# Kernel tuning notes

Hardware: AMD Instinct MI355X
Metric: run time of the kernel (lower is better)

## Reference

```python
import jax, jax.numpy as jnp
import numpy as np

B, S, E, H = 8, 2048, 384, 6
D = E // H  # head dim = 64


def setup_inputs() -> dict:
    key = jax.random.key(0)
    ks = jax.random.split(key, 5)
    s = 1.0 / np.sqrt(E)
    return {
        "x": jax.random.normal(ks[0], (B, S, E), dtype=jnp.float32),
        "Wq": jax.random.normal(ks[1], (E, E), dtype=jnp.float32) * s,
        "Wk": jax.random.normal(ks[2], (E, E), dtype=jnp.float32) * s,
        "Wv": jax.random.normal(ks[3], (E, E), dtype=jnp.float32) * s,
        "Wo": jax.random.normal(ks[4], (E, E), dtype=jnp.float32) * s,
        "bo": jnp.zeros((E,), dtype=jnp.float32),
    }


def reference(x, Wq, Wk, Wv, Wo, bo):
    b, s, e = x.shape
    # QKV projections (torch Linear with bias=False: x @ W.T; here W stored as [in,out])
    q = (x @ Wq).reshape(b, s, H, D).transpose(0, 2, 1, 3)  # [b,h,s,d]
    k = (x @ Wk).reshape(b, s, H, D).transpose(0, 2, 1, 3)
    v = (x @ Wv).reshape(b, s, H, D).transpose(0, 2, 1, 3)
    scores = jnp.einsum("bhqd,bhkd->bhqk", q, k) / jnp.sqrt(jnp.asarray(D, x.dtype))
    causal = jnp.tril(jnp.ones((s, s), dtype=bool))
    scores = jnp.where(causal, scores, -jnp.inf)
    attn = jax.nn.softmax(scores, axis=-1)
    # NOTE: original applies dropout but then uses the PRE-dropout softmax for @V,
    # so dropout is a no-op; we faithfully omit it.
    out = jnp.einsum("bhqk,bhkd->bhqd", attn, v)  # [b,h,s,d]
    out = out.transpose(0, 2, 1, 3).reshape(b, s, e)
    return out @ Wo + bo
```

## Files before the change

kernel.cpp:

```cpp
#include <hip/hip_runtime.h>
#include <hip/hip_bf16.h>
#include <cstdint>
#include <cstddef>

typedef __attribute__((ext_vector_type(8))) short short8;
typedef __attribute__((ext_vector_type(4))) float f32x4;

#define S_LEN 2048
#define EMB 384
#define NH 6
#define HD 64
#define NB 8
#define QSCALE 0.180336880f

__device__ __forceinline__ unsigned short f2bf(float f) {
  return __builtin_bit_cast(unsigned short, __float2bfloat16(f));
}

__global__ __launch_bounds__(256) void k_prep(
    const float* __restrict__ x, unsigned short* __restrict__ xb,
    const float* __restrict__ Wq, const float* __restrict__ Wk,
    const float* __restrict__ Wv, const float* __restrict__ Wo,
    unsigned short* __restrict__ Wqt, unsigned short* __restrict__ Wkt,
    unsigned short* __restrict__ Wvt, unsigned short* __restrict__ Wot) {
  const int tid = threadIdx.x;
  if (blockIdx.x < 1536) {
    int i = blockIdx.x * 256 + tid;
    const int n4 = (NB * S_LEN * EMB) / 4;
    for (; i < n4; i += 1536 * 256) {
      const float4 v = reinterpret_cast<const float4*>(x)[i];
      ushort4 o;
      o.x = f2bf(v.x); o.y = f2bf(v.y); o.z = f2bf(v.z); o.w = f2bf(v.w);
      reinterpret_cast<ushort4*>(xb)[i] = o;
    }
  } else {
    __shared__ unsigned short Lw[64 * 66];
    const int bx2 = blockIdx.x - 1536;
    const int mat = bx2 / 36;
    const int tile = bx2 - mat * 36;
    const int k0 = (tile / 6) * 64;
    const int n0 = (tile % 6) * 64;
    const float* W = (mat == 0) ? Wq : (mat == 1) ? Wk : (mat == 2) ? Wv : Wo;
    unsigned short* Wt = (mat == 0) ? Wqt : (mat == 1) ? Wkt : (mat == 2) ? Wvt : Wot;
    const int f4 = tid & 15;
#pragma unroll
    for (int it = 0; it < 4; ++it) {
      const int kl = it * 16 + (tid >> 4);
      const float4 v = reinterpret_cast<const float4*>(W + (size_t)(k0 + kl) * EMB + n0)[f4];
      Lw[kl * 66 + f4 * 4 + 0] = f2bf(v.x);
      Lw[kl * 66 + f4 * 4 + 1] = f2bf(v.y);
      Lw[kl * 66 + f4 * 4 + 2] = f2bf(v.z);
      Lw[kl * 66 + f4 * 4 + 3] = f2bf(v.w);
    }
    __syncthreads();
    const int g = tid & 7;
#pragma unroll
    for (int it = 0; it < 2; ++it) {
      const int nl = it * 32 + (tid >> 3);
      short8 o;
#pragma unroll
      for (int j = 0; j < 8; ++j) o[j] = (short)Lw[(g * 8 + j) * 66 + nl];
      *reinterpret_cast<short8*>(Wt + (size_t)(n0 + nl) * EMB + k0 + g * 8) = o;
    }
  }
}

__global__ __launch_bounds__(256) void k_qkv(
    const unsigned short* __restrict__ xb,
    const unsigned short* __restrict__ Wqt,
    const unsigned short* __restrict__ Wkt,
    const unsigned short* __restrict__ Wvt,
    unsigned short* __restrict__ Qb,
    unsigned short* __restrict__ Kb,
    unsigned short* __restrict__ Vtb) {
  __shared__ __attribute__((aligned(16))) unsigned short La[128 * 72];
  __shared__ __attribute__((aligned(16))) unsigned short Lt[64 * 136];

  const int tid = threadIdx.x;
  const int lane = tid & 63;
  const int w = tid >> 6;
  const int wr = w >> 1, wc = w & 1;
  const int lr = lane & 15, lg = lane >> 4;

  const int bid = blockIdx.y * 128 + blockIdx.x;
  const int xcd = bid & 7;
  const int pos = bid >> 3;
  const int bx = xcd * 16 + (pos & 15);
  const int by = pos >> 4;
  const int m0 = bx * 128;
  const int wsel = by / 3;
  const int n0 = (by % 3) * 128;
  const unsigned short* Wt = (wsel == 0) ? Wqt : (wsel == 1) ? Wkt : Wvt;

  const int srow = tid >> 3;
  const int sg = tid & 7;

  f32x4 acc[4][4] = {};
  short8 st[4];
  short8 breg[2][2][4];

#pragma unroll
  for (int i = 0; i < 4; ++i)
    st[i] = *reinterpret_cast<const short8*>(
        xb + (size_t)(m0 + i * 32 + srow) * EMB + sg * 8);
#pragma unroll
  for (int kk = 0; kk < 2; ++kk)
#pragma unroll
    for (int ns = 0; ns < 4; ++ns)
      breg[0][kk][ns] = *reinterpret_cast<const short8*>(
          Wt + (size_t)(n0 + wc * 64 + ns * 16 + lr) * EMB + kk * 32 + lg * 8);

#pragma unroll
  for (int kt = 0; kt < 6; ++kt) {
    const int cur = kt & 1, nxt = cur ^ 1;
    __syncthreads();
#pragma unroll
    for (int i = 0; i < 4; ++i)
      *reinterpret_cast<short8*>(&La[(i * 32 + srow) * 72 + sg * 8]) = st[i];
    __syncthreads();
    if (kt < 5) {
      const int kn = (kt + 1) * 64;
#pragma unroll
      for (int i = 0; i < 4; ++i)
        st[i] = *reinterpret_cast<const short8*>(
            xb + (size_t)(m0 + i * 32 + srow) * EMB + kn + sg * 8);
#pragma unroll
      for (int kk = 0; kk < 2; ++kk)
#pragma unroll
        for (int ns = 0; ns < 4; ++ns)
          breg[nxt][kk][ns] = *reinterpret_cast<const short8*>(
              Wt + (size_t)(n0 + wc * 64 + ns * 16 + lr) * EMB + kn + kk * 32 + lg * 8);
    }
#pragma unroll
    for (int kk = 0; kk < 2; ++kk) {
      short8 a[4];
#pragma unroll
      for (int ms = 0; ms < 4; ++ms)
        a[ms] = *reinterpret_cast<const short8*>(
            &La[(wr * 64 + ms * 16 + lr) * 72 + kk * 32 + lg * 8]);
#pragma unroll
      for (int ms = 0; ms < 4; ++ms)
#pragma unroll
        for (int ns = 0; ns < 4; ++ns)
          acc[ms][ns] = __builtin_amdgcn_mfma_f32_16x16x32_bf16(
              a[ms], breg[cur][kk][ns], acc[ms][ns], 0, 0, 0);
    }
  }

  if (wsel != 2) {
    unsigned short* Out = (wsel == 0) ? Qb : Kb;
    const float sc = (wsel == 0) ? QSCALE : 1.0f;
#pragma unroll
    for (int ms = 0; ms < 4; ++ms)
#pragma unroll
      for (int ns = 0; ns < 4; ++ns)
#pragma unroll
        for (int r = 0; r < 4; ++r) {
          const int m = m0 + wr * 64 + ms * 16 + lg * 4 + r;
          const int n = n0 + wc * 64 + ns * 16 + lr;
          const int bb = m >> 11;
          const int s = m & 2047;
          const int h = n >> 6;
          const int d = n & 63;
          Out[(((size_t)bb * NH + h) * S_LEN + s) * HD + d] = f2bf(acc[ms][ns][r] * sc);
        }
  } else {
    const int bb = m0 >> 11;
    const int s0 = m0 & 2047;
#pragma unroll
    for (int p = 0; p < 2; ++p) {
      __syncthreads();
      if (wc == p) {
#pragma unroll
        for (int ms = 0; ms < 4; ++ms)
#pragma unroll
          for (int ns = 0; ns < 4; ++ns)
#pragma unroll
            for (int r = 0; r < 4; ++r) {
              const int dl = ns * 16 + lr;
              const int ml = wr * 64 + ms * 16 + lg * 4 + r;
              Lt[dl * 136 + (((ml >> 3) ^ (dl & 7)) << 3) + (ml & 7)] = f2bf(acc[ms][ns][r]);
            }
      }
      __syncthreads();
      const int hg = 2 * (n0 >> 7) + p;
      const int c = tid & 15;
#pragma unroll
      for (int it = 0; it < 4; ++it) {
        const int d = it * 16 + (tid >> 4);
        const short8 v = *reinterpret_cast<const short8*>(
            &Lt[d * 136 + ((c ^ (d & 7)) << 3)]);
        *reinterpret_cast<short8*>(
            Vtb + (((size_t)bb * NH + hg) * HD + d) * S_LEN + s0 + c * 8) = v;
      }
    }
  }
}

__global__ __launch_bounds__(256) void k_attn(
    const unsigned short* __restrict__ Qb,
    const unsigned short* __restrict__ Kb,
    const unsigned short* __restrict__ Vtg,
    unsigned short* __restrict__ Ob) {
  __shared__ __attribute__((aligned(16))) unsigned short Ks[64 * 64];
  __shared__ __attribute__((aligned(16))) unsigned short Vt[64 * 64];
  __shared__ __attribute__((aligned(16))) unsigned short Ps[64 * 64];

  const int tid = threadIdx.x;
  const int lane = tid & 63;
  const int w = tid >> 6;
  const int lr = lane & 15, lg = lane >> 4;

  const int lin = blockIdx.y * 16 + blockIdx.x;
  const int swz = (lin & 7) * 96 + (lin >> 3);
  const int pair = swz & 15;
  const int bh = swz >> 4;

  const unsigned short* Qp = Qb + (size_t)bh * S_LEN * HD;
  const unsigned short* Kp = Kb + (size_t)bh * S_LEN * HD;
  const unsigned short* Vp = Vtg + (size_t)bh * S_LEN * HD;
  const int b = bh / NH, hh = bh - b * NH;

  const int srow = tid >> 3;
  const int sslot = tid & 7;
  const int wsl0 = (sslot ^ (srow & 7)) << 3;

  for (int phase = 0; phase < 2; ++phase) {
    const int qt = phase ? (31 - pair) : pair;
    const int qbase = qt * 64 + w * 16;

    const short8 aq0 = *reinterpret_cast<const short8*>(Qp + (size_t)(qbase + lr) * HD + lg * 8);
    const short8 aq1 = *reinterpret_cast<const short8*>(Qp + (size_t)(qbase + lr) * HD + 32 + lg * 8);

    f32x4 o[4] = {};
    float l_i[4] = {0.f, 0.f, 0.f, 0.f};

    short8 pk0 = *reinterpret_cast<const short8*>(Kp + (size_t)srow * HD + sslot * 8);
    short8 pk1 = *reinterpret_cast<const short8*>(Kp + (size_t)(srow + 32) * HD + sslot * 8);
    short8 pv0 = *reinterpret_cast<const short8*>(Vp + (size_t)srow * S_LEN + sslot * 8);
    short8 pv1 = *reinterpret_cast<const short8*>(Vp + (size_t)(srow + 32) * S_LEN + sslot * 8);

    for (int t = 0; t <= qt; ++t) {
      __syncthreads();
      *reinterpret_cast<short8*>(&Ks[srow * 64 + wsl0]) = pk0;
      *reinterpret_cast<short8*>(&Ks[(srow + 32) * 64 + wsl0]) = pk1;
      *reinterpret_cast<short8*>(&Vt[srow * 64 + wsl0]) = pv0;
      *reinterpret_cast<short8*>(&Vt[(srow + 32) * 64 + wsl0]) = pv1;
      __syncthreads();

      if (t < qt) {
        const int tn = (t + 1) * 64;
        pk0 = *reinterpret_cast<const short8*>(Kp + (size_t)(tn + srow) * HD + sslot * 8);
        pk1 = *reinterpret_cast<const short8*>(Kp + (size_t)(tn + srow + 32) * HD + sslot * 8);
        pv0 = *reinterpret_cast<const short8*>(Vp + (size_t)srow * S_LEN + tn + sslot * 8);
        pv1 = *reinterpret_cast<const short8*>(Vp + (size_t)(srow + 32) * S_LEN + tn + sslot * 8);
      }

      float sv[4][4];
#pragma unroll
      for (int ks = 0; ks < 4; ++ks) {
        const int kstart = t * 64 + ks * 16;
        if (kstart > qbase + 15) {
#pragma unroll
          for (int r = 0; r < 4; ++r) sv[ks][r] = -1e30f;
        } else {
          const int krow = ks * 16 + lr;
          const int kx = krow & 7;
          const short8 bk0 = *reinterpret_cast<const short8*>(&Ks[krow * 64 + ((lg ^ kx) << 3)]);
          const short8 bk1 = *reinterpret_cast<const short8*>(&Ks[krow * 64 + (((4 + lg) ^ kx) << 3)]);
          f32x4 s = {};
          s = __builtin_amdgcn_mfma_f32_16x16x32_bf16(aq0, bk0, s, 0, 0, 0);
          s = __builtin_amdgcn_mfma_f32_16x16x32_bf16(aq1, bk1, s, 0, 0, 0);
          if (kstart + 15 <= qbase) {
#pragma unroll
            for (int r = 0; r < 4; ++r) sv[ks][r] = s[r];
          } else {
            const int kg = kstart + lr;
#pragma unroll
            for (int r = 0; r < 4; ++r)
              sv[ks][r] = (kg <= qbase + lg * 4 + r) ? s[r] : -1e30f;
          }
        }
      }

#pragma unroll
      for (int r = 0; r < 4; ++r) {
        const int q = w * 16 + lg * 4 + r;
        const int qx = q & 7;
        const int abase = q * 64 + (lr & 7);
        const int sp = lr >> 3;
        float p[4];
#pragma unroll
        for (int ks = 0; ks < 4; ++ks) p[ks] = __builtin_amdgcn_exp2f(sv[ks][r]);
        l_i[r] += (p[0] + p[1]) + (p[2] + p[3]);
#pragma unroll
        for (int ks = 0; ks < 4; ++ks)
          Ps[abase + ((((ks << 1) | sp) ^ qx) << 3)] = f2bf(p[ks]);
      }

      const int qrow = w * 16 + lr;
      const int qx2 = qrow & 7;
#pragma unroll
      for (int kk = 0; kk < 2; ++kk) {
        const short8 ap = *reinterpret_cast<const short8*>(
            &Ps[qrow * 64 + (((kk * 4 + lg) ^ qx2) << 3)]);
#pragma unroll
        for (int ns = 0; ns < 4; ++ns) {
          const int vrow = ns * 16 + lr;
          const short8 bv = *reinterpret_cast<const short8*>(
              &Vt[vrow * 64 + (((kk * 4 + lg) ^ (vrow & 7)) << 3)]);
          o[ns] = __builtin_amdgcn_mfma_f32_16x16x32_bf16(ap, bv, o[ns], 0, 0, 0);
        }
      }
    }

#pragma unroll
    for (int r = 0; r < 4; ++r) {
      float l = l_i[r];
      l += __shfl_xor(l, 1);
      l += __shfl_xor(l, 2);
      l += __shfl_xor(l, 4);
      l += __shfl_xor(l, 8);
      l_i[r] = 1.0f / l;
    }
#pragma unroll
    for (int ns = 0; ns < 4; ++ns)
#pragma unroll
      for (int r = 0; r < 4; ++r) {
        const int qg = qbase + lg * 4 + r;
        const float val = o[ns][r] * l_i[r];
        Ob[((size_t)(b * S_LEN + qg)) * EMB + hh * HD + ns * 16 + lr] = f2bf(val);
      }
  }
}

__global__ __launch_bounds__(256) void k_oproj(
    const unsigned short* __restrict__ Ob,
    const unsigned short* __restrict__ Wot,
    const float* __restrict__ bo,
    float* __restrict__ out) {
  __shared__ __attribute__((aligned(16))) unsigned short La[64 * 72];

  const int tid = threadIdx.x;
  const int lane = tid & 63;
  const int w = tid >> 6;
  const int lr = lane & 15, lg = lane >> 4;

  const int bid = blockIdx.y * 256 + blockIdx.x;
  const int xcd = bid & 7;
  const int pos = bid >> 3;
  const int m0 = (xcd * 32 + (pos & 31)) * 64;
  const int n0 = (pos >> 5) * 128;

  const int srow = tid >> 3;
  const int sg = tid & 7;

  f32x4 acc[4][2] = {};
  short8 st[2];
  short8 breg[2][2][2];

#pragma unroll
  for (int i = 0; i < 2; ++i)
    st[i] = *reinterpret_cast<const short8*>(
        Ob + (size_t)(m0 + i * 32 + srow) * EMB + sg * 8);
#pragma unroll
  for (int kk = 0; kk < 2; ++kk)
#pragma unroll
    for (int ns = 0; ns < 2; ++ns)
      breg[0][kk][ns] = *reinterpret_cast<const short8*>(
          Wot + (size_t)(n0 + w * 32 + ns * 16 + lr) * EMB + kk * 32 + lg * 8);

#pragma unroll
  for (int kt = 0; kt < 6; ++kt) {
    const int cur = kt & 1, nxt = cur ^ 1;
    __syncthreads();
#pragma unroll
    for (int i = 0; i < 2; ++i)
      *reinterpret_cast<short8*>(&La[(i * 32 + srow) * 72 + sg * 8]) = st[i];
    __syncthreads();
    if (kt < 5) {
      const int kn = (kt + 1) * 64;
#pragma unroll
      for (int i = 0; i < 2; ++i)
        st[i] = *reinterpret_cast<const short8*>(
            Ob + (size_t)(m0 + i * 32 + srow) * EMB + kn + sg * 8);
#pragma unroll
      for (int kk = 0; kk < 2; ++kk)
#pragma unroll
        for (int ns = 0; ns < 2; ++ns)
          breg[nxt][kk][ns] = *reinterpret_cast<const short8*>(
              Wot + (size_t)(n0 + w * 32 + ns * 16 + lr) * EMB + kn + kk * 32 + lg * 8);
    }
#pragma unroll
    for (int kk = 0; kk < 2; ++kk) {
      short8 a[4];
#pragma unroll
      for (int ms = 0; ms < 4; ++ms)
        a[ms] = *reinterpret_cast<const short8*>(
            &La[(ms * 16 + lr) * 72 + kk * 32 + lg * 8]);
#pragma unroll
      for (int ms = 0; ms < 4; ++ms)
#pragma unroll
        for (int ns = 0; ns < 2; ++ns)
          acc[ms][ns] = __builtin_amdgcn_mfma_f32_16x16x32_bf16(
              a[ms], breg[cur][kk][ns], acc[ms][ns], 0, 0, 0);
    }
  }

#pragma unroll
  for (int ms = 0; ms < 4; ++ms)
#pragma unroll
    for (int ns = 0; ns < 2; ++ns)
#pragma unroll
      for (int r = 0; r < 4; ++r) {
        const int m = m0 + ms * 16 + lg * 4 + r;
        const int n = n0 + w * 32 + ns * 16 + lr;
        out[(size_t)m * EMB + n] = acc[ms][ns][r] + bo[n];
      }
}

extern "C" void kernel_launch(void* const* d_in, const int* in_sizes, int n_in,
                              void* d_out, int out_size, void* d_ws, size_t ws_size,
                              hipStream_t stream) {
  const float* x  = (const float*)d_in[0];
  const float* Wq = (const float*)d_in[1];
  const float* Wk = (const float*)d_in[2];
  const float* Wv = (const float*)d_in[3];
  const float* Wo = (const float*)d_in[4];
  const float* bo = (const float*)d_in[5];
  float* out = (float*)d_out;

  uint8_t* ws = (uint8_t*)d_ws;
  unsigned short* xb  = (unsigned short*)(ws);
  unsigned short* Wqt = (unsigned short*)(ws + 12582912);
  unsigned short* Wkt = (unsigned short*)(ws + 12877824);
  unsigned short* Wvt = (unsigned short*)(ws + 13172736);
  unsigned short* Wot = (unsigned short*)(ws + 13467648);
  unsigned short* Qb  = (unsigned short*)(ws + 13762560);
  unsigned short* Kb  = (unsigned short*)(ws + 26345472);
  unsigned short* VT  = (unsigned short*)(ws + 38928384);
  unsigned short* Ob  = (unsigned short*)(ws + 51511296);

  hipLaunchKernelGGL(k_prep, dim3(1680), dim3(256), 0, stream,
                     x, xb, Wq, Wk, Wv, Wo, Wqt, Wkt, Wvt, Wot);
  hipLaunchKernelGGL(k_qkv, dim3(128, 9), dim3(256), 0, stream,
                     xb, Wqt, Wkt, Wvt, Qb, Kb, VT);
  hipLaunchKernelGGL(k_attn, dim3(16, 48), dim3(256), 0, stream, Qb, Kb, VT, Ob);
  hipLaunchKernelGGL(k_oproj, dim3(256, 3), dim3(256), 0, stream, Ob, Wot, bo, out);
}
```

Measured before the change: 197.8 us.

## Fuse x bf16 conversion into QKV GEMM and stage epilogue stores through LDS

Removes the separate pass that converted x to bf16 into a workspace buffer. The QKV GEMM now loads fp32 x directly and converts it while staging into LDS, and the prep kernel only transposes the weights. The Q/K epilogue and the output projection epilogue now write through shared memory so each thread issues wide, coalesced vector stores instead of scattered scalar ones. In exchange, fp32 x is re-read by each of the 9 column blocks, which doubles the bytes per load, and the extra LDS buffer in k_oproj may lower occupancy.

```diff
diff --git a/kernel.cpp b/kernel.cpp
--- a/kernel.cpp
+++ b/kernel.cpp
@@ -17,56 +17,44 @@
   return __builtin_bit_cast(unsigned short, __float2bfloat16(f));
 }
 
-__global__ __launch_bounds__(256) void k_prep(
-    const float* __restrict__ x, unsigned short* __restrict__ xb,
+__global__ __launch_bounds__(256) void k_prepw(
     const float* __restrict__ Wq, const float* __restrict__ Wk,
     const float* __restrict__ Wv, const float* __restrict__ Wo,
     unsigned short* __restrict__ Wqt, unsigned short* __restrict__ Wkt,
     unsigned short* __restrict__ Wvt, unsigned short* __restrict__ Wot) {
+  __shared__ unsigned short Lw[64 * 66];
   const int tid = threadIdx.x;
-  if (blockIdx.x < 1536) {
-    int i = blockIdx.x * 256 + tid;
-    const int n4 = (NB * S_LEN * EMB) / 4;
-    for (; i < n4; i += 1536 * 256) {
-      const float4 v = reinterpret_cast<const float4*>(x)[i];
-      ushort4 o;
-      o.x = f2bf(v.x); o.y = f2bf(v.y); o.z = f2bf(v.z); o.w = f2bf(v.w);
-      reinterpret_cast<ushort4*>(xb)[i] = o;
-    }
-  } else {
-    __shared__ unsigned short Lw[64 * 66];
-    const int bx2 = blockIdx.x - 1536;
-    const int mat = bx2 / 36;
-    const int tile = bx2 - mat * 36;
-    const int k0 = (tile / 6) * 64;
-    const int n0 = (tile % 6) * 64;
-    const float* W = (mat == 0) ? Wq : (mat == 1) ? Wk : (mat == 2) ? Wv : Wo;
-    unsigned short* Wt = (mat == 0) ? Wqt : (mat == 1) ? Wkt : (mat == 2) ? Wvt : Wot;
-    const int f4 = tid & 15;
-#pragma unroll
-    for (int it = 0; it < 4; ++it) {
-      const int kl = it * 16 + (tid >> 4);
-      const float4 v = reinterpret_cast<const float4*>(W + (size_t)(k0 + kl) * EMB + n0)[f4];
-      Lw[kl * 66 + f4 * 4 + 0] = f2bf(v.x);
-      Lw[kl * 66 + f4 * 4 + 1] = f2bf(v.y);
-      Lw[kl * 66 + f4 * 4 + 2] = f2bf(v.z);
-      Lw[kl * 66 + f4 * 4 + 3] = f2bf(v.w);
-    }
-    __syncthreads();
-    const int g = tid & 7;
-#pragma unroll
-    for (int it = 0; it < 2; ++it) {
-      const int nl = it * 32 + (tid >> 3);
-      short8 o;
-#pragma unroll
-      for (int j = 0; j < 8; ++j) o[j] = (short)Lw[(g * 8 + j) * 66 + nl];
-      *reinterpret_cast<short8*>(Wt + (size_t)(n0 + nl) * EMB + k0 + g * 8) = o;
-    }
+  const int bx2 = blockIdx.x;
+  const int mat = bx2 / 36;
+  const int tile = bx2 - mat * 36;
+  const int k0 = (tile / 6) * 64;
+  const int n0 = (tile % 6) * 64;
+  const float* W = (mat == 0) ? Wq : (mat == 1) ? Wk : (mat == 2) ? Wv : Wo;
+  unsigned short* Wt = (mat == 0) ? Wqt : (mat == 1) ? Wkt : (mat == 2) ? Wvt : Wot;
+  const int f4 = tid & 15;
+#pragma unroll
+  for (int it = 0; it < 4; ++it) {
+    const int kl = it * 16 + (tid >> 4);
+    const float4 v = reinterpret_cast<const float4*>(W + (size_t)(k0 + kl) * EMB + n0)[f4];
+    Lw[kl * 66 + f4 * 4 + 0] = f2bf(v.x);
+    Lw[kl * 66 + f4 * 4 + 1] = f2bf(v.y);
+    Lw[kl * 66 + f4 * 4 + 2] = f2bf(v.z);
+    Lw[kl * 66 + f4 * 4 + 3] = f2bf(v.w);
+  }
+  __syncthreads();
+  const int g = tid & 7;
+#pragma unroll
+  for (int it = 0; it < 2; ++it) {
+    const int nl = it * 32 + (tid >> 3);
+    short8 o;
+#pragma unroll
+    for (int j = 0; j < 8; ++j) o[j] = (short)Lw[(g * 8 + j) * 66 + nl];
+    *reinterpret_cast<short8*>(Wt + (size_t)(n0 + nl) * EMB + k0 + g * 8) = o;
   }
 }
 
 __global__ __launch_bounds__(256) void k_qkv(
-    const unsigned short* __restrict__ xb,
+    const float* __restrict__ x,
     const unsigned short* __restrict__ Wqt,
     const unsigned short* __restrict__ Wkt,
     const unsigned short* __restrict__ Wvt,
@@ -96,13 +84,15 @@
   const int sg = tid & 7;
 
   f32x4 acc[4][4] = {};
-  short8 st[4];
+  float4 xf[4][2];
   short8 breg[2][2][4];
 
 #pragma unroll
-  for (int i = 0; i < 4; ++i)
-    st[i] = *reinterpret_cast<const short8*>(
-        xb + (size_t)(m0 + i * 32 + srow) * EMB + sg * 8);
+  for (int i = 0; i < 4; ++i) {
+    const float* src = x + (size_t)(m0 + i * 32 + srow) * EMB + sg * 8;
+    xf[i][0] = *reinterpret_cast<const float4*>(src);
+    xf[i][1] = *reinterpret_cast<const float4*>(src + 4);
+  }
 #pragma unroll
   for (int kk = 0; kk < 2; ++kk)
 #pragma unroll
@@ -115,15 +105,23 @@
     const int cur = kt & 1, nxt = cur ^ 1;
     __syncthreads();
 #pragma unroll
-    for (int i = 0; i < 4; ++i)
-      *reinterpret_cast<short8*>(&La[(i * 32 + srow) * 72 + sg * 8]) = st[i];
+    for (int i = 0; i < 4; ++i) {
+      short8 v;
+      v[0] = (short)f2bf(xf[i][0].x); v[1] = (short)f2bf(xf[i][0].y);
+      v[2] = (short)f2bf(xf[i][0].z); v[3] = (short)f2bf(xf[i][0].w);
+      v[4] = (short)f2bf(xf[i][1].x); v[5] = (short)f2bf(xf[i][1].y);
+      v[6] = (short)f2bf(xf[i][1].z); v[7] = (short)f2bf(xf[i][1].w);
+      *reinterpret_cast<short8*>(&La[(i * 32 + srow) * 72 + sg * 8]) = v;
+    }
     __syncthreads();
     if (kt < 5) {
       const int kn = (kt + 1) * 64;
 #pragma unroll
-      for (int i = 0; i < 4; ++i)
-        st[i] = *reinterpret_cast<const short8*>(
-            xb + (size_t)(m0 + i * 32 + srow) * EMB + kn + sg * 8);
+      for (int i = 0; i < 4; ++i) {
+        const float* src = x + (size_t)(m0 + i * 32 + srow) * EMB + kn + sg * 8;
+        xf[i][0] = *reinterpret_cast<const float4*>(src);
+        xf[i][1] = *reinterpret_cast<const float4*>(src + 4);
+      }
 #pragma unroll
       for (int kk = 0; kk < 2; ++kk)
 #pragma unroll
@@ -147,26 +145,37 @@
     }
   }
 
+  const int bb = m0 >> 11;
+  const int s0 = m0 & 2047;
   if (wsel != 2) {
     unsigned short* Out = (wsel == 0) ? Qb : Kb;
     const float sc = (wsel == 0) ? QSCALE : 1.0f;
 #pragma unroll
-    for (int ms = 0; ms < 4; ++ms)
-#pragma unroll
-      for (int ns = 0; ns < 4; ++ns)
-#pragma unroll
-        for (int r = 0; r < 4; ++r) {
-          const int m = m0 + wr * 64 + ms * 16 + lg * 4 + r;
-          const int n = n0 + wc * 64 + ns * 16 + lr;
-          const int bb = m >> 11;
-          const int s = m & 2047;
-          const int h = n >> 6;
-          const int d = n & 63;
-          Out[(((size_t)bb * NH + h) * S_LEN + s) * HD + d] = f2bf(acc[ms][ns][r] * sc);
-        }
+    for (int p = 0; p < 2; ++p) {
+      __syncthreads();
+      if (wr == p) {
+#pragma unroll
+        for (int ms = 0; ms < 4; ++ms)
+#pragma unroll
+          for (int ns = 0; ns < 4; ++ns)
+#pragma unroll
+            for (int r = 0; r < 4; ++r)
+              Lt[(ms * 16 + lg * 4 + r) * 136 + wc * 64 + ns * 16 + lr] =
+                  f2bf(acc[ms][ns][r] * sc);
+      }
+      __syncthreads();
+#pragma unroll
+      for (int it = 0; it < 4; ++it) {
+        const int row = (tid >> 3) + 32 * (it & 1);
+        const int ch = (tid & 7) + 8 * (it >> 1);
+        const short8 v = *reinterpret_cast<const short8*>(&Lt[row * 136 + ch * 8]);
+        const int n = n0 + ch * 8;
+        const int h = n >> 6, d = n & 63;
+        *reinterpret_cast<short8*>(
+            Out + (((size_t)bb * NH + h) * S_LEN + (s0 + p * 64 + row)) * HD + d) = v;
+      }
+    }
   } else {
-    const int bb = m0 >> 11;
-    const int s0 = m0 & 2047;
 #pragma unroll
     for (int p = 0; p < 2; ++p) {
       __syncthreads();
@@ -340,6 +349,7 @@
     const float* __restrict__ bo,
     float* __restrict__ out) {
   __shared__ __attribute__((aligned(16))) unsigned short La[64 * 72];
+  __shared__ __attribute__((aligned(16))) float Lf[64 * 132];
 
   const int tid = threadIdx.x;
   const int lane = tid & 63;
@@ -407,16 +417,24 @@
     }
   }
 
+  __syncthreads();
 #pragma unroll
   for (int ms = 0; ms < 4; ++ms)
 #pragma unroll
     for (int ns = 0; ns < 2; ++ns)
 #pragma unroll
-      for (int r = 0; r < 4; ++r) {
-        const int m = m0 + ms * 16 + lg * 4 + r;
-        const int n = n0 + w * 32 + ns * 16 + lr;
-        out[(size_t)m * EMB + n] = acc[ms][ns][r] + bo[n];
-      }
+      for (int r = 0; r < 4; ++r)
+        Lf[(ms * 16 + lg * 4 + r) * 132 + w * 32 + ns * 16 + lr] = acc[ms][ns][r];
+  __syncthreads();
+#pragma unroll
+  for (int it = 0; it < 8; ++it) {
+    const int row = (tid >> 3) + 32 * (it & 1);
+    const int c4 = (tid & 7) + 8 * (it >> 1);
+    float4 v = *reinterpret_cast<const float4*>(&Lf[row * 132 + c4 * 4]);
+    const float4 b4 = *reinterpret_cast<const float4*>(&bo[n0 + c4 * 4]);
+    v.x += b4.x; v.y += b4.y; v.z += b4.z; v.w += b4.w;
+    *reinterpret_cast<float4*>(&out[(size_t)(m0 + row) * EMB + n0 + c4 * 4]) = v;
+  }
 }
 
 extern "C" void kernel_launch(void* const* d_in, const int* in_sizes, int n_in,
@@ -431,7 +449,6 @@
   float* out = (float*)d_out;
 
   uint8_t* ws = (uint8_t*)d_ws;
-  unsigned short* xb  = (unsigned short*)(ws);
   unsigned short* Wqt = (unsigned short*)(ws + 12582912);
   unsigned short* Wkt = (unsigned short*)(ws + 12877824);
   unsigned short* Wvt = (unsigned short*)(ws + 13172736);
@@ -441,10 +458,10 @@
   unsigned short* VT  = (unsigned short*)(ws + 38928384);
   unsigned short* Ob  = (unsigned short*)(ws + 51511296);
 
-  hipLaunchKernelGGL(k_prep, dim3(1680), dim3(256), 0, stream,
-                     x, xb, Wq, Wk, Wv, Wo, Wqt, Wkt, Wvt, Wot);
+  hipLaunchKernelGGL(k_prepw, dim3(144), dim3(256), 0, stream,
+                     Wq, Wk, Wv, Wo, Wqt, Wkt, Wvt, Wot);
   hipLaunchKernelGGL(k_qkv, dim3(128, 9), dim3(256), 0, stream,
-                     xb, Wqt, Wkt, Wvt, Qb, Kb, VT);
+                     x, Wqt, Wkt, Wvt, Qb, Kb, VT);
   hipLaunchKernelGGL(k_attn, dim3(16, 48), dim3(256), 0, stream, Qb, Kb, VT, Ob);
   hipLaunchKernelGGL(k_oproj, dim3(256, 3), dim3(256), 0, stream, Ob, Wot, bo, out);
 }
```

New measurement: 202.2 us. 2.2% more time.
